# Kernel optimization log

Hardware: AMD Instinct MI355X
Metric: run time of the kernel (lower is better)

The kernel has to match this reference:

```python
import jax, jax.numpy as jnp
import numpy as np

DROP_PROB = 0.1
BLOCK_SIZE = 7  # odd -> no even-size trim branch
N, C, H, W = 64, 256, 28, 28


def conv3x3(x, w):
    # x: [N,C,H,W], w: [O,I,3,3], stride 1, SAME padding
    return jax.lax.conv_general_dilated(
        x, w, window_strides=(1, 1), padding='SAME',
        dimension_numbers=('NCHW', 'OIHW', 'NCHW'))


def setup_inputs() -> dict:
    key = jax.random.key(0)
    k1, k2, k3, k4 = jax.random.split(key, 4)
    x = jax.random.normal(k1, (N, C, H, W), jnp.float32)
    # learned conv weights for the two branches (layer3 and premodel.layer3)
    w_layer3 = jax.random.normal(k2, (C, C, 3, 3), jnp.float32) * 0.05
    w_pre = jax.random.normal(k3, (C, C, 3, 3), jnp.float32) * 0.05
    # uniform draws used for the Bernoulli(gamma) drop mask, shape (N,H,W)
    mask_u = jax.random.uniform(k4, (N, H, W), jnp.float32)
    return {'x': x, 'w_layer3': w_layer3, 'w_pre': w_pre, 'mask_u': mask_u}


def reference(x, w_layer3, w_pre, mask_u):
    gamma = DROP_PROB / (BLOCK_SIZE ** 2)
    a = conv3x3(x, w_layer3)   # x = self.layer3(x)
    b = conv3x3(x, w_pre)      # output4 = self.premodel.layer3(x)
    # mask = (rand(N,H,W) < gamma).float()
    mask = (mask_u < gamma).astype(x.dtype)  # [N,H,W]
    # block_mask = 1 - max_pool2d(mask, k=block_size, stride=1, pad=block_size//2)
    pooled = jax.lax.reduce_window(
        mask, -jnp.inf, jax.lax.max,
        window_dimensions=(1, BLOCK_SIZE, BLOCK_SIZE),
        window_strides=(1, 1, 1), padding='SAME')
    block_mask = 1.0 - pooled  # [N,H,W]
    # fused blend: keep layer3 output where block_mask==1, else premodel output
    out = jnp.where(block_mask[:, None, :, :] == 1.0, a, b)  # [N,C,H,W]
    # out * block_mask.numel() / block_mask.sum()
    scale = jnp.asarray(block_mask.size, x.dtype) / jnp.sum(block_mask)
    return out * scale
```

## Files before the change

### kernel.cpp

```cpp
#include <hip/hip_runtime.h>
#include <hip/hip_bf16.h>


typedef __bf16  bf16x8 __attribute__((ext_vector_type(8)));
typedef float   f32x4  __attribute__((ext_vector_type(4)));
typedef short   short8 __attribute__((ext_vector_type(8)));
typedef unsigned int u32;
typedef unsigned short u16;

#define XT_OFF     65536
#define WT_OFF     29556736
#define LISTA_OFF  31916032
#define LISTB_OFF  32116736
#define SLOT       22528

__device__ __forceinline__ u16 f2bf(float v) {
    u32 u = __float_as_uint(v);
    u32 r = (u + 0x7FFFu + ((u >> 16) & 1u)) >> 16;
    return (u16)r;
}

__device__ __forceinline__ void gll16(const void* g, void* l) {
    __builtin_amdgcn_global_load_lds(
        (const __attribute__((address_space(1))) u32*)g,
        (__attribute__((address_space(3))) u32*)l, 16, 0, 0);
}

__global__ void prep_kernel(const float* __restrict__ x,
                            const float* __restrict__ wl,
                            const float* __restrict__ wp,
                            const float* __restrict__ mu,
                            u16* __restrict__ xt, u16* __restrict__ wt,
                            int* __restrict__ listA, int* __restrict__ listB,
                            int* __restrict__ cntB, int* __restrict__ cntA) {
    int b = blockIdx.x, tid = threadIdx.x;
    if (b < 1920) {
        int n = b / 30, oh = b % 30;
        u16* row = xt + (size_t)(n * 30 + oh) * 30 * 256;
        if (oh == 0 || oh == 29) {
            u32* r32 = (u32*)row;
            #pragma unroll
            for (int i = 0; i < 15; ++i) r32[i * 256 + tid] = 0;
            return;
        }
        __shared__ u16 sm[7168];
        int h = oh - 1;
        const float* src = x + ((size_t)(n * 256 + tid) * 28 + h) * 28;
        float f[28];
        #pragma unroll
        for (int q = 0; q < 7; ++q) {
            float4 v = *(const float4*)(src + q * 4);
            f[q * 4 + 0] = v.x; f[q * 4 + 1] = v.y;
            f[q * 4 + 2] = v.z; f[q * 4 + 3] = v.w;
        }
        #pragma unroll
        for (int w = 0; w < 28; ++w)
            sm[w * 256 + tid] = f2bf(f[w]);
        __syncthreads();
        u32* r32 = (u32*)row;
        if (tid < 128) r32[tid] = 0;
        else           r32[29 * 128 + (tid - 128)] = 0;
        const u32* s32 = (const u32*)sm;
        u32* dst = r32 + 128;
        #pragma unroll
        for (int k = 0; k < 14; ++k)
            dst[k * 256 + tid] = s32[k * 256 + tid];
    } else if (b < 2496) {
        int gid = (b - 1920) * 256 + tid;
        int base = gid << 3;
        int bb = base >> 12;
        int e = base & 4095;
        int t = bb >> 2, nq = bb & 3;
        int kk = t >> 3;
        int row = e >> 5, ps = (e & 31) >> 3;
        int c0 = (t & 7) * 32 + ((ps ^ ((row >> 1) & 3)) << 3);
        int o = nq * 128 + row;
        const float* wsrc = (o < 256) ? wl : wp;
        const float* wr = wsrc + ((size_t)(o & 255) * 256 + c0) * 9 + kk;
        short8 v;
        #pragma unroll
        for (int j = 0; j < 8; ++j) v[j] = (short)f2bf(wr[j * 9]);
        *(short8*)(wt + base) = v;
    } else {
        __shared__ int lsum[4];
        __shared__ int basB, basA;
        int m = (b - 2496) * 256 + tid;
        int n = m / 784, rem = m % 784;
        int h = rem / 28, w = rem % 28;
        const float g = (float)(0.1 / 49.0);
        const float* un = mu + n * 784;
        int p = 0;
        for (int dy = -3; dy <= 3; ++dy) {
            int hh = h + dy;
            if (hh < 0 || hh >= 28) continue;
            for (int dx = -3; dx <= 3; ++dx) {
                int ww = w + dx;
                if (ww < 0 || ww >= 28) continue;
                p |= (un[hh * 28 + ww] < g) ? 1 : 0;
            }
        }
        unsigned long long ball = __ballot(p);
        int wid = tid >> 6, ln = tid & 63;
        if (ln == 0) lsum[wid] = __popcll(ball);
        __syncthreads();
        if (tid == 0) {
            int tB = lsum[0] + lsum[1] + lsum[2] + lsum[3];
            basB = atomicAdd(cntB, tB);
            basA = atomicAdd(cntA, 256 - tB);
        }
        __syncthreads();
        int offB = 0, offA = 0;
        for (int i = 0; i < wid; ++i) { offB += lsum[i]; offA += 64 - lsum[i]; }
        int rank1 = __popcll(ball & ((1ULL << ln) - 1));
        int rank0 = ln - rank1;
        if (p) listB[basB + offB + rank1] = m;
        else   listA[basA + offA + rank0] = m;
    }
}

__global__ __launch_bounds__(256, 2)
void conv_kernel(const char* __restrict__ xt,
                 const char* __restrict__ wt,
                 const int* __restrict__ listA,
                 const int* __restrict__ listB,
                 const int* __restrict__ dropped,
                 float* __restrict__ out) {
    __shared__ char smem[55296];
    const int tid = threadIdx.x;
    const int lb = (blockIdx.x & 7) * 57 + (blockIdx.x >> 3);
    const int vt = lb >> 1;
    const int nh = lb & 1;
    const int cB = *dropped;
    const int cA = 50176 - cB;
    const int naT = (cA + 223) / 224;
    const int nbT = (cB + 223) / 224;
    if (vt >= naT + nbT) return;
    const int branch = (vt >= naT) ? 1 : 0;
    const int tix = branch ? (vt - naT) : vt;
    const int cnt = branch ? cB : cA;
    const int* lst = branch ? listB : listA;
    const int nq = branch * 2 + nh;
    const int lane = tid & 63, wave = tid >> 6;
    const int lane15 = lane & 15, grp = lane >> 4;
    const int wm = wave >> 1, wn = wave & 1;

    long pbA[4];
    {
        int swz = ((tid & 3) ^ ((tid >> 3) & 3)) << 4;
        #pragma unroll
        for (int i = 0; i < 4; ++i) {
            int r = i * 64 + (tid >> 2);
            int idx = tix * 224 + r;
            if (idx >= cnt) idx = cnt - 1;
            int m = lst[idx];
            int n = m / 784, rem = m % 784;
            pbA[i] = (long)(((n * 30 + rem / 28 + 1) * 30 + (rem % 28 + 1)) * 512
                            + swz);
        }
    }

    f32x4 acc[7][4];
    #pragma unroll
    for (int i = 0; i < 7; ++i)
        #pragma unroll
        for (int j = 0; j < 4; ++j)
            acc[i][j] = (f32x4){0.f, 0.f, 0.f, 0.f};

    const int so  = (grp ^ ((lane15 >> 1) & 3)) << 4;
    const int arb = wm * 7168 + (lane15 << 6) + so;
    const int brb = 14336 + wn * 4096 + (lane15 << 6) + so;

#define AON(TC) ((long)((TC) >> 3) / 3 * 15360 + (long)(((TC) >> 3) % 3) * 512 \
                 - 15872 + (long)(((TC) & 7) << 6))
#define STG(TC, SL) { char* sd_ = smem + (SL) * SLOT;                       \
        const long ao_ = AON(TC);                                           \
        gll16(xt + pbA[0] + ao_, sd_ + (tid << 4));                         \
        gll16(xt + pbA[1] + ao_, sd_ + 4096 + (tid << 4));                  \
        gll16(xt + pbA[2] + ao_, sd_ + 8192 + (tid << 4));                  \
        if (tid < 128) gll16(xt + pbA[3] + ao_, sd_ + 12288 + (tid << 4));  \
        const char* wb_ = wt + ((size_t)((TC) * 4 + nq) << 13);             \
        gll16(wb_ + (tid << 4), sd_ + 14336 + (tid << 4));                  \
        gll16(wb_ + 4096 + (tid << 4), sd_ + 18432 + (tid << 4)); }
#define DS_AV0(dst, SL) { const char* sb_ = smem + (SL) * SLOT;             \
        _Pragma("unroll")                                                   \
        for (int fm = 0; fm < 4; ++fm)                                      \
            dst[fm] = *(const bf16x8*)(sb_ + arb + (fm << 10)); }
#define DS_AV1(dst, SL) { const char* sb_ = smem + (SL) * SLOT + 4096;      \
        _Pragma("unroll")                                                   \
        for (int fm = 0; fm < 3; ++fm)                                      \
            dst[fm] = *(const bf16x8*)(sb_ + arb + (fm << 10)); }
#define DS_BV(dst, SL) { const char* sb_ = smem + (SL) * SLOT;              \
        _Pragma("unroll")                                                   \
        for (int fn = 0; fn < 4; ++fn)                                      \
            dst[fn] = *(const bf16x8*)(sb_ + brb + (fn << 10)); }
#define MM(A0_, NF, AV, BV) { __builtin_amdgcn_s_setprio(1);                \
        _Pragma("unroll")                                                   \
        for (int fm = 0; fm < (NF); ++fm)                                   \
            _Pragma("unroll")                                               \
            for (int fn = 0; fn < 4; ++fn)                                  \
                acc[(A0_)+fm][fn] = __builtin_amdgcn_mfma_f32_16x16x32_bf16( \
                    AV[fm], BV[fn], acc[(A0_)+fm][fn], 0, 0, 0);            \
        __builtin_amdgcn_s_setprio(0); }
#define LGKM(N) { asm volatile("s_waitcnt lgkmcnt(" #N ")" ::: "memory");   \
                  __builtin_amdgcn_sched_barrier(0); }
#define VM0     { asm volatile("s_waitcnt vmcnt(0)" ::: "memory");          \
                  __builtin_amdgcn_sched_barrier(0); }
#define BAR     asm volatile("s_barrier" ::: "memory")

    bf16x8 av0[4], av1[3], bv[4];

    STG(0, 0);
    VM0;
    BAR;

    for (int t = 0; t < 72; ++t) {
        const int sc = t & 1, ss = sc ^ 1;
        if (t < 71) STG(t + 1, ss);
        DS_AV0(av0, sc);
        DS_BV(bv, sc);
        DS_AV1(av1, sc);
        LGKM(3);
        MM(0, 4, av0, bv);
        LGKM(0);
        MM(4, 3, av1, bv);
        VM0;
        BAR;
    }

    float scale = 50176.0f / (float)(50176 - cB);
    float* ep = (float*)smem + wave * 2080;
    __syncthreads();
    #pragma unroll
    for (int rr = 0; rr < 4; ++rr) {
        const int r2 = rr & 1;
        const int mh = rr >> 1;
        const int nf = mh ? 3 : 4;
        for (int fm2 = 0; fm2 < nf; ++fm2)
            #pragma unroll
            for (int f2 = 0; f2 < 2; ++f2)
                #pragma unroll
                for (int j = 0; j < 4; ++j)
                    ep[(f2 * 16 + lane15) * 65 + fm2 * 16 + grp * 4 + j] =
                        acc[mh * 4 + fm2][r2 * 2 + f2][j];
        __syncthreads();
        {
            int gidx = tix * 224 + wm * 112 + mh * 64 + lane;
            if ((mh == 0 || lane < 48) && gidx < cnt) {
                int m = lst[gidx];
                int n = m / 784, rem = m % 784;
                size_t ob = (size_t)n * 200704 + rem;
                #pragma unroll
                for (int ch = 0; ch < 32; ++ch) {
                    int c = nh * 128 + wn * 64 + r2 * 32 + ch;
                    out[ob + (size_t)c * 784] = ep[ch * 65 + lane] * scale;
                }
            }
        }
        __syncthreads();
    }
#undef AON
#undef STG
#undef DS_AV0
#undef DS_AV1
#undef DS_BV
#undef MM
#undef LGKM
#undef VM0
#undef BAR
}

extern "C" void kernel_launch(void* const* d_in, const int* in_sizes, int n_in,
                              void* d_out, int out_size, void* d_ws, size_t ws_size,
                              hipStream_t stream) {
    const float* x  = (const float*)d_in[0];
    const float* wl = (const float*)d_in[1];
    const float* wp = (const float*)d_in[2];
    const float* mu = (const float*)d_in[3];
    float* out = (float*)d_out;
    char* ws = (char*)d_ws;

    int* cntB = (int*)ws;
    int* cntA = (int*)(ws + 4);
    u16* xt = (u16*)(ws + XT_OFF);
    u16* wt = (u16*)(ws + WT_OFF);
    int* listA = (int*)(ws + LISTA_OFF);
    int* listB = (int*)(ws + LISTB_OFF);

    hipMemsetAsync(ws, 0, 8, stream);

    prep_kernel<<<2692, 256, 0, stream>>>(x, wl, wp, mu, xt, wt,
                                          listA, listB, cntB, cntA);
    conv_kernel<<<456, 256, 0, stream>>>((const char*)xt, (const char*)wt,
                                         listA, listB, cntB, out);
}
```

Baseline: 103.2 us.

## Shrink conv tile to 128 pixels with two-wave blocks and more workgroups

Changes the conv workgroup from four waves covering 224 pixels × 128 channels to two waves covering 128 pixels × 128 channels. Each wave now owns 64 pixels across all 128 channels. The grid grows from 456 to 800 blocks, LDS per block drops, and the pixel-tail waste from 224-sized tiles shrinks. In exchange there is less weight reuse per staged tile, each block issues more global-to-LDS loads per thread, and per-CU wave count may be lower.

```diff
diff --git a/kernel.cpp b/kernel.cpp
--- a/kernel.cpp
+++ b/kernel.cpp
@@ -12,7 +12,7 @@
 #define WT_OFF     29556736
 #define LISTA_OFF  31916032
 #define LISTB_OFF  32116736
-#define SLOT       22528
+#define SLOT       16384
 
 __device__ __forceinline__ u16 f2bf(float v) {
     u32 u = __float_as_uint(v);
@@ -118,22 +118,22 @@
     }
 }
 
-__global__ __launch_bounds__(256, 2)
+__global__ __launch_bounds__(128, 2)
 void conv_kernel(const char* __restrict__ xt,
                  const char* __restrict__ wt,
                  const int* __restrict__ listA,
                  const int* __restrict__ listB,
                  const int* __restrict__ dropped,
                  float* __restrict__ out) {
-    __shared__ char smem[55296];
+    __shared__ char smem[32768];
     const int tid = threadIdx.x;
-    const int lb = (blockIdx.x & 7) * 57 + (blockIdx.x >> 3);
+    const int lb = (blockIdx.x & 7) * 100 + (blockIdx.x >> 3);
     const int vt = lb >> 1;
     const int nh = lb & 1;
     const int cB = *dropped;
     const int cA = 50176 - cB;
-    const int naT = (cA + 223) / 224;
-    const int nbT = (cB + 223) / 224;
+    const int naT = (cA + 127) >> 7;
+    const int nbT = (cB + 127) >> 7;
     if (vt >= naT + nbT) return;
     const int branch = (vt >= naT) ? 1 : 0;
     const int tix = branch ? (vt - naT) : vt;
@@ -142,15 +142,13 @@
     const int nq = branch * 2 + nh;
     const int lane = tid & 63, wave = tid >> 6;
     const int lane15 = lane & 15, grp = lane >> 4;
-    const int wm = wave >> 1, wn = wave & 1;
 
     long pbA[4];
     {
         int swz = ((tid & 3) ^ ((tid >> 3) & 3)) << 4;
         #pragma unroll
         for (int i = 0; i < 4; ++i) {
-            int r = i * 64 + (tid >> 2);
-            int idx = tix * 224 + r;
+            int idx = tix * 128 + i * 32 + (tid >> 2);
             if (idx >= cnt) idx = cnt - 1;
             int m = lst[idx];
             int n = m / 784, rem = m % 784;
@@ -159,47 +157,45 @@
         }
     }
 
-    f32x4 acc[7][4];
+    f32x4 acc[4][8];
     #pragma unroll
-    for (int i = 0; i < 7; ++i)
-        #pragma unroll
-        for (int j = 0; j < 4; ++j)
+    for (int i = 0; i < 4; ++i)
+        #pragma unroll
+        for (int j = 0; j < 8; ++j)
             acc[i][j] = (f32x4){0.f, 0.f, 0.f, 0.f};
 
     const int so  = (grp ^ ((lane15 >> 1) & 3)) << 4;
-    const int arb = wm * 7168 + (lane15 << 6) + so;
-    const int brb = 14336 + wn * 4096 + (lane15 << 6) + so;
+    const int arb = wave * 4096 + (lane15 << 6) + so;
+    const int brb = 8192 + (lane15 << 6) + so;
 
 #define AON(TC) ((long)((TC) >> 3) / 3 * 15360 + (long)(((TC) >> 3) % 3) * 512 \
                  - 15872 + (long)(((TC) & 7) << 6))
 #define STG(TC, SL) { char* sd_ = smem + (SL) * SLOT;                       \
         const long ao_ = AON(TC);                                           \
         gll16(xt + pbA[0] + ao_, sd_ + (tid << 4));                         \
-        gll16(xt + pbA[1] + ao_, sd_ + 4096 + (tid << 4));                  \
-        gll16(xt + pbA[2] + ao_, sd_ + 8192 + (tid << 4));                  \
-        if (tid < 128) gll16(xt + pbA[3] + ao_, sd_ + 12288 + (tid << 4));  \
+        gll16(xt + pbA[1] + ao_, sd_ + 2048 + (tid << 4));                  \
+        gll16(xt + pbA[2] + ao_, sd_ + 4096 + (tid << 4));                  \
+        gll16(xt + pbA[3] + ao_, sd_ + 6144 + (tid << 4));                  \
         const char* wb_ = wt + ((size_t)((TC) * 4 + nq) << 13);             \
-        gll16(wb_ + (tid << 4), sd_ + 14336 + (tid << 4));                  \
-        gll16(wb_ + 4096 + (tid << 4), sd_ + 18432 + (tid << 4)); }
-#define DS_AV0(dst, SL) { const char* sb_ = smem + (SL) * SLOT;             \
+        gll16(wb_ + (tid << 4), sd_ + 8192 + (tid << 4));                   \
+        gll16(wb_ + 2048 + (tid << 4), sd_ + 10240 + (tid << 4));           \
+        gll16(wb_ + 4096 + (tid << 4), sd_ + 12288 + (tid << 4));           \
+        gll16(wb_ + 6144 + (tid << 4), sd_ + 14336 + (tid << 4)); }
+#define DS_A(dst, SL) { const char* sb_ = smem + (SL) * SLOT;               \
         _Pragma("unroll")                                                   \
         for (int fm = 0; fm < 4; ++fm)                                      \
             dst[fm] = *(const bf16x8*)(sb_ + arb + (fm << 10)); }
-#define DS_AV1(dst, SL) { const char* sb_ = smem + (SL) * SLOT + 4096;      \
+#define DS_B(dst, SL) { const char* sb_ = smem + (SL) * SLOT;               \
         _Pragma("unroll")                                                   \
-        for (int fm = 0; fm < 3; ++fm)                                      \
-            dst[fm] = *(const bf16x8*)(sb_ + arb + (fm << 10)); }
-#define DS_BV(dst, SL) { const char* sb_ = smem + (SL) * SLOT;              \
+        for (int fn = 0; fn < 8; ++fn)                                      \
+            dst[fn] = *(const bf16x8*)(sb_ + brb + (fn << 10)); }
+#define MM(F0, F1, AV, BV) { __builtin_amdgcn_s_setprio(1);                 \
         _Pragma("unroll")                                                   \
-        for (int fn = 0; fn < 4; ++fn)                                      \
-            dst[fn] = *(const bf16x8*)(sb_ + brb + (fn << 10)); }
-#define MM(A0_, NF, AV, BV) { __builtin_amdgcn_s_setprio(1);                \
-        _Pragma("unroll")                                                   \
-        for (int fm = 0; fm < (NF); ++fm)                                   \
+        for (int fm = 0; fm < 4; ++fm)                                      \
             _Pragma("unroll")                                               \
-            for (int fn = 0; fn < 4; ++fn)                                  \
-                acc[(A0_)+fm][fn] = __builtin_amdgcn_mfma_f32_16x16x32_bf16( \
-                    AV[fm], BV[fn], acc[(A0_)+fm][fn], 0, 0, 0);            \
+            for (int fn = (F0); fn < (F1); ++fn)                            \
+                acc[fm][fn] = __builtin_amdgcn_mfma_f32_16x16x32_bf16(      \
+                    AV[fm], BV[fn], acc[fm][fn], 0, 0, 0);                  \
         __builtin_amdgcn_s_setprio(0); }
 #define LGKM(N) { asm volatile("s_waitcnt lgkmcnt(" #N ")" ::: "memory");   \
                   __builtin_amdgcn_sched_barrier(0); }
@@ -207,7 +203,7 @@
                   __builtin_amdgcn_sched_barrier(0); }
 #define BAR     asm volatile("s_barrier" ::: "memory")
 
-    bf16x8 av0[4], av1[3], bv[4];
+    bf16x8 av[4], bv[8];
 
     STG(0, 0);
     VM0;
@@ -216,13 +212,12 @@
     for (int t = 0; t < 72; ++t) {
         const int sc = t & 1, ss = sc ^ 1;
         if (t < 71) STG(t + 1, ss);
-        DS_AV0(av0, sc);
-        DS_BV(bv, sc);
-        DS_AV1(av1, sc);
-        LGKM(3);
-        MM(0, 4, av0, bv);
+        DS_A(av, sc);
+        DS_B(bv, sc);
+        LGKM(4);
+        MM(0, 4, av, bv);
         LGKM(0);
-        MM(4, 3, av1, bv);
+        MM(4, 8, av, bv);
         VM0;
         BAR;
     }
@@ -230,39 +225,34 @@
     float scale = 50176.0f / (float)(50176 - cB);
     float* ep = (float*)smem + wave * 2080;
     __syncthreads();
+    const int gidx = tix * 128 + wave * 64 + lane;
     #pragma unroll
-    for (int rr = 0; rr < 4; ++rr) {
-        const int r2 = rr & 1;
-        const int mh = rr >> 1;
-        const int nf = mh ? 3 : 4;
-        for (int fm2 = 0; fm2 < nf; ++fm2)
+    for (int np = 0; np < 4; ++np) {
+        #pragma unroll
+        for (int fm2 = 0; fm2 < 4; ++fm2)
             #pragma unroll
-            for (int f2 = 0; f2 < 2; ++f2)
+            for (int fp = 0; fp < 2; ++fp)
                 #pragma unroll
                 for (int j = 0; j < 4; ++j)
-                    ep[(f2 * 16 + lane15) * 65 + fm2 * 16 + grp * 4 + j] =
-                        acc[mh * 4 + fm2][r2 * 2 + f2][j];
-        __syncthreads();
-        {
-            int gidx = tix * 224 + wm * 112 + mh * 64 + lane;
-            if ((mh == 0 || lane < 48) && gidx < cnt) {
-                int m = lst[gidx];
-                int n = m / 784, rem = m % 784;
-                size_t ob = (size_t)n * 200704 + rem;
-                #pragma unroll
-                for (int ch = 0; ch < 32; ++ch) {
-                    int c = nh * 128 + wn * 64 + r2 * 32 + ch;
-                    out[ob + (size_t)c * 784] = ep[ch * 65 + lane] * scale;
-                }
+                    ep[(fp * 16 + lane15) * 65 + fm2 * 16 + grp * 4 + j] =
+                        acc[fm2][np * 2 + fp][j];
+        __syncthreads();
+        if (gidx < cnt) {
+            int m = lst[gidx];
+            int n = m / 784, rem = m % 784;
+            size_t ob = (size_t)n * 200704 + rem;
+            #pragma unroll
+            for (int ch = 0; ch < 32; ++ch) {
+                int c = nh * 128 + np * 32 + ch;
+                out[ob + (size_t)c * 784] = ep[ch * 65 + lane] * scale;
             }
         }
         __syncthreads();
     }
 #undef AON
 #undef STG
-#undef DS_AV0
-#undef DS_AV1
-#undef DS_BV
+#undef DS_A
+#undef DS_B
 #undef MM
 #undef LGKM
 #undef VM0
@@ -290,6 +280,6 @@
 
     prep_kernel<<<2692, 256, 0, stream>>>(x, wl, wp, mu, xt, wt,
                                           listA, listB, cntB, cntA);
-    conv_kernel<<<456, 256, 0, stream>>>((const char*)xt, (const char*)wt,
+    conv_kernel<<<800, 128, 0, stream>>>((const char*)xt, (const char*)wt,
                                          listA, listB, cntB, out);
 }
```

Result: slower. 109.7 us (+6.3%).
